# Kernel tuning notes

Measured on AMD Instinct MI355X. Metric: run time of the kernel, lower is better.

## Reference

```python
import jax, jax.numpy as jnp
import numpy as np

D_MODEL = 768; HEADS = 8; LAYERS = 2

def pos_encoding(n, d):
    pos = np.arange(n, dtype=np.float32)[:, None]
    div = np.exp(np.arange(0, d, 2, dtype=np.float32) * -(np.log(10000.0) / d))
    pe = np.zeros((n, d), np.float32)
    pe[:, 0::2] = np.sin(pos * div)
    pe[:, 1::2] = np.cos(pos * div)
    return jnp.asarray(pe)

def layer_norm(x, g, b):
    m = x.mean(-1, keepdims=True)
    v = ((x - m) ** 2).mean(-1, keepdims=True)
    return (x - m) / jnp.sqrt(v + 1e-6) * g + b

def mha(k_in, v_in, q_in, mask, Wq, bq, Wk, bk, Wv, bv, Wout, bout):
    # BertSum MultiHeadedAttention(key, value, query, mask); mask True = blocked
    B, Lq, d = q_in.shape
    dk = d // HEADS
    def proj(x, W, b):
        y = x @ W + b
        return y.reshape(B, x.shape[1], HEADS, dk).transpose(0, 2, 1, 3)
    q = proj(q_in, Wq, bq)
    k = proj(k_in, Wk, bk)
    v = proj(v_in, Wv, bv)
    scores = jnp.einsum('bhqd,bhkd->bhqk', q, k) / jnp.sqrt(jnp.float32(dk))
    scores = jnp.where(mask[:, None, :, :], jnp.float32(-1e18), scores)
    attn = jax.nn.softmax(scores, axis=-1)
    out = jnp.einsum('bhqk,bhkd->bhqd', attn, v).transpose(0, 2, 1, 3).reshape(B, Lq, d)
    return out @ Wout + bout

def ffn(x, W1, b1, W2, b2, g, b):
    # PositionwiseFeedForward: x + w2(gelu(w1(LN(x))))
    return x + jax.nn.gelu(layer_norm(x, g, b) @ W1 + b1) @ W2 + b2

def setup_inputs():
    key = jax.random.key(0)
    ks = jax.random.split(key, 20)
    B, N_TOP, N_OUT, D, DFF, DH = 8, 512, 64, D_MODEL, 3072, 512
    s = 0.02
    return {
        'top_vecs': jax.random.normal(ks[0], (B, N_TOP, D), jnp.float32),
        'inputs': jax.random.normal(ks[1], (B, N_OUT, D), jnp.float32),
        'mask': jnp.ones((B, N_TOP), bool),
        'label_mask': jnp.ones((B, N_OUT), bool),
        'Wq': jax.random.normal(ks[2], (LAYERS, D, D)) * s,
        'bq': jnp.zeros((LAYERS, D)),
        'Wk': jax.random.normal(ks[3], (LAYERS, D, D)) * s,
        'bk': jnp.zeros((LAYERS, D)),
        'Wv': jax.random.normal(ks[4], (LAYERS, D, D)) * s,
        'bv': jnp.zeros((LAYERS, D)),
        'Wout': jax.random.normal(ks[5], (LAYERS, D, D)) * s,
        'bout': jnp.zeros((LAYERS, D)),
        'W1': jax.random.normal(ks[6], (LAYERS, D, DFF)) * s,
        'b1': jnp.zeros((LAYERS, DFF)),
        'W2': jax.random.normal(ks[7], (LAYERS, DFF, D)) * s,
        'b2': jnp.zeros((LAYERS, D)),
        'ln_g': jnp.ones((LAYERS, D)),
        'ln_b': jnp.zeros((LAYERS, D)),
        'Wo': jax.random.normal(ks[8], (D, DH)) * s,
        'bo': jnp.zeros((DH,)),
        'Wi': jax.random.normal(ks[9], (D, DH)) * s,
        'bi': jnp.zeros((DH,)),
        'v_w': jax.random.normal(ks[10], (DH,)) * s,
        'v_b': jnp.zeros(()),
    }

def reference(top_vecs, inputs, mask, label_mask, Wq, bq, Wk, bk, Wv, bv, Wout, bout,
              W1, b1, W2, b2, ln_g, ln_b, Wo, bo, Wi, bi, v_w, v_b):
    B, n_out, d = inputs.shape
    pe = pos_encoding(n_out, d)
    seq_mask = jnp.triu(jnp.ones((n_out, n_out), bool), 1)  # future positions blocked
    self_mask = (~label_mask)[:, None, :] | seq_mask[None]  # (B, n_out, n_out)
    ctx_mask = jnp.broadcast_to((~mask)[:, None, :], (B, n_out, mask.shape[1]))
    x = inputs + pe[None]
    for i in range(LAYERS):
        ctx = mha(x, x, x, self_mask, Wq[i], bq[i], Wk[i], bk[i], Wv[i], bv[i], Wout[i], bout[i])
        dec = mha(top_vecs, top_vecs, ctx, ctx_mask, Wq[i], bq[i], Wk[i], bk[i], Wv[i], bv[i], Wout[i], bout[i])
        x = ffn(dec, W1[i], b1[i], W2[i], b2[i], ln_g[i], ln_b[i])
    # additive-attention scoring head: (B, n_out, n_top, d_hidden) broadcast intermediate
    h = jax.nn.leaky_relu((x @ Wo + bo)[:, :, None, :] + (top_vecs @ Wi + bi)[:, None, :, :])
    scores = jnp.einsum('bonh,h->bon', h, v_w) + v_b
    return jax.nn.softmax(scores, axis=-1)
```

## Files before the change

kernel.cpp:

```cpp
#include <hip/hip_runtime.h>
#include <math.h>

#define D_MODEL 768
#define HEADS   8
#define DK      96
#define NB      8
#define N_TOP   512
#define N_OUT   64
#define DFF     3072
#define DH      512

typedef short  short8  __attribute__((ext_vector_type(8)));
typedef float  floatx4 __attribute__((ext_vector_type(4)));

__device__ __forceinline__ unsigned short f2bf(float f) {
    unsigned int u = __float_as_uint(f);
    u += 0x7fffu + ((u >> 16) & 1u);
    return (unsigned short)(u >> 16);
}
__device__ __forceinline__ float bf2f(unsigned short h) {
    return __uint_as_float(((unsigned int)h) << 16);
}

__device__ __forceinline__ float gelu_f(float x) {
    const float c = 0.7978845608028654f;
    return 0.5f * x * (1.0f + tanhf(c * (x + 0.044715f * x * x * x)));
}

__device__ __forceinline__ void gl16(const short* g, short* l) {
    __builtin_amdgcn_global_load_lds(
        (const __attribute__((address_space(1))) void*)g,
        (__attribute__((address_space(3))) void*)l, 16, 0, 0);
}

__device__ __forceinline__ float block_reduce_sum(float v, float* red) {
    int tid = threadIdx.x;
    red[tid] = v;
    __syncthreads();
    for (int s = blockDim.x >> 1; s > 0; s >>= 1) {
        if (tid < s) red[tid] += red[tid + s];
        __syncthreads();
    }
    float r = red[0];
    __syncthreads();
    return r;
}
__device__ __forceinline__ float block_reduce_max(float v, float* red) {
    int tid = threadIdx.x;
    red[tid] = v;
    __syncthreads();
    for (int s = blockDim.x >> 1; s > 0; s >>= 1) {
        if (tid < s) red[tid] = fmaxf(red[tid], red[tid + s]);
        __syncthreads();
    }
    float r = red[0];
    __syncthreads();
    return r;
}

struct TPack {
    const float* src[14];
    short*       dst[14];
    int K[14], N[14];
    int tstart[15];
};

__global__ __launch_bounds__(256) void multi_transpose_kernel(TPack pk) {
    __shared__ float t[32][33];
    int tile = blockIdx.x;
    int i = 0;
    while (i < 13 && tile >= pk.tstart[i + 1]) ++i;
    int lt = tile - pk.tstart[i];
    int K = pk.K[i], N = pk.N[i];
    int ntx = N >> 5;
    int bx = lt % ntx, by = lt / ntx;
    const float* in = pk.src[i];
    short* out = pk.dst[i];
    int tx = threadIdx.x & 31, ty = threadIdx.x >> 5;
#pragma unroll
    for (int r = 0; r < 4; ++r)
        t[ty + r * 8][tx] = in[(size_t)(by * 32 + ty + r * 8) * N + bx * 32 + tx];
    __syncthreads();
#pragma unroll
    for (int r = 0; r < 4; ++r)
        out[(size_t)(bx * 32 + ty + r * 8) * K + by * 32 + tx] =
            (short)f2bf(t[tx][ty + r * 8]);
}

__global__ void convert_bf16_kernel(const float* __restrict__ in, short* __restrict__ out, int n4) {
    int i = blockIdx.x * blockDim.x + threadIdx.x;
    if (i >= n4) return;
    float4 v = ((const float4*)in)[i];
    out[i * 4 + 0] = (short)f2bf(v.x);
    out[i * 4 + 1] = (short)f2bf(v.y);
    out[i * 4 + 2] = (short)f2bf(v.z);
    out[i * 4 + 3] = (short)f2bf(v.w);
}

__global__ void add_pe_kernel(const float* __restrict__ in, short* __restrict__ xb, int total) {
    int idx = blockIdx.x * blockDim.x + threadIdx.x;
    if (idx >= total) return;
    int c   = idx % D_MODEL;
    int pos = (idx / D_MODEL) % N_OUT;
    int j   = c >> 1;
    float ang = (float)pos * expf((float)(2 * j) * (-logf(10000.0f) / (float)D_MODEL));
    float pe  = (c & 1) ? cosf(ang) : sinf(ang);
    xb[idx] = (short)f2bf(in[idx] + pe);
}

struct GDesc {
    const short* A;
    const short* Bt;
    int K;
    int nbx;
    short*       dst[3];
    const float* bias[3];
    int cum[4];
    int vtlog[3];
    int nseg;
};
struct GPack {
    GDesc d[3];
    int start1, start2;
};

__global__ __launch_bounds__(256) void gemm128g_kernel(GPack gp) {
    __shared__ __align__(16) short As[3 * 128 * 32];
    __shared__ __align__(16) short Bs[3 * 128 * 32];

    const int nwg = gridDim.x, orig = blockIdx.x;
    const int q8 = nwg >> 3, r8 = nwg & 7, xcd = orig & 7, loc = orig >> 3;
    const int blk = (xcd < r8 ? xcd * (q8 + 1) : r8 * (q8 + 1) + (xcd - r8) * q8) + loc;

    const int di = (blk >= gp.start1 ? 1 : 0) + (blk >= gp.start2 ? 1 : 0);
    const GDesc& D = gp.d[di];
    const int l = blk - (di == 0 ? 0 : (di == 1 ? gp.start1 : gp.start2));
    const int bm = (l / D.nbx) * 128, bn = (l % D.nbx) * 128;
    const int K = D.K;
    const int nst = K >> 5;

    const int tid  = threadIdx.x;
    const int wave = tid >> 6, lane = tid & 63;
    const int wr = wave >> 1, wc = wave & 1;
    const int lc = lane & 15;
    const int lq = lane >> 4;
    const int lr4 = lq * 4;
    const int ko  = (lq ^ ((lc >> 1) & 3)) * 8;

    const int srow = wave * 32 + (lane >> 2);
    const int scol = ((lane & 3) ^ ((lane >> 3) & 3)) * 8;
    const int sbase = wave * 1024;

    floatx4 acc[4][4];
#pragma unroll
    for (int i = 0; i < 4; ++i)
#pragma unroll
        for (int j = 0; j < 4; ++j) acc[i][j] = (floatx4)0.0f;

    const short* Ab = D.A  + (size_t)(bm + srow) * K + scol;
    const short* Bb = D.Bt + (size_t)(bn + srow) * K + scol;
    const size_t hq = (size_t)16 * K;

#define STG128(t, buf) do {                                   \
        const short* _a = Ab + (size_t)(t) * 32;              \
        const short* _b = Bb + (size_t)(t) * 32;              \
        short* _la = As + (buf) * 4096 + sbase;               \
        short* _lb = Bs + (buf) * 4096 + sbase;               \
        gl16(_a,      _la);                                   \
        gl16(_a + hq, _la + 512);                             \
        gl16(_b,      _lb);                                   \
        gl16(_b + hq, _lb + 512);                             \
    } while (0)

    STG128(0, 0);
    if (nst > 1) {
        STG128(1, 1);
        asm volatile("s_waitcnt vmcnt(4)" ::: "memory");
    } else {
        asm volatile("s_waitcnt vmcnt(0)" ::: "memory");
    }
    __builtin_amdgcn_s_barrier();

    int cur = 0;
    for (int t = 0; t < nst; ++t) {
        int pre = cur + 2; if (pre >= 3) pre -= 3;
        const bool more = (t + 2) < nst;
        if (more) STG128(t + 2, pre);
        const short* Ar = As + cur * 4096;
        const short* Br = Bs + cur * 4096;
        short8 a[4], b[4];
#pragma unroll
        for (int f = 0; f < 4; ++f) {
            a[f] = *(const short8*)&Ar[(wr * 64 + f * 16 + lc) * 32 + ko];
            b[f] = *(const short8*)&Br[(wc * 64 + f * 16 + lc) * 32 + ko];
        }
#pragma unroll
        for (int fr = 0; fr < 4; ++fr)
#pragma unroll
            for (int fc = 0; fc < 4; ++fc)
                acc[fr][fc] = __builtin_amdgcn_mfma_f32_16x16x32_bf16(
                    a[fr], b[fc], acc[fr][fc], 0, 0, 0);
        if (more) asm volatile("s_waitcnt vmcnt(4)" ::: "memory");
        else      asm volatile("s_waitcnt vmcnt(0)" ::: "memory");
        __builtin_amdgcn_s_barrier();
        if (++cur == 3) cur = 0;
    }
#undef STG128

#pragma unroll
    for (int fc = 0; fc < 4; ++fc) {
        int col = bn + wc * 64 + fc * 16 + lc;
        int s = 0;
        while (s + 1 < D.nseg && col >= D.cum[s + 1]) ++s;
        int cl   = col - D.cum[s];
        int segw = D.cum[s + 1] - D.cum[s];
        const float* bp = D.bias[s];
        short* dst = D.dst[s];
        int vtl = D.vtlog[s];
        float bi = bp ? bp[cl] : 0.0f;
#pragma unroll
        for (int fr = 0; fr < 4; ++fr)
#pragma unroll
            for (int r = 0; r < 4; ++r) {
                int row = bm + wr * 64 + fr * 16 + lr4 + r;
                float x = acc[fr][fc][r] + bi;
                if (vtl) {
                    int seq = 1 << vtl;
                    dst[((size_t)(row >> vtl) * segw + cl) * seq + (row & (seq - 1))] =
                        (short)f2bf(x);
                } else {
                    dst[(size_t)row * segw + cl] = (short)f2bf(x);
                }
            }
    }
}

__global__ __launch_bounds__(256) void gemm_bf16_kernel(
    const short* __restrict__ A, const short* __restrict__ Bt,
    const float* __restrict__ bias0, const float* __restrict__ bias1,
    const float* __restrict__ bias2, const float* __restrict__ residual,
    float* __restrict__ Cf, short* __restrict__ Cb0, short* __restrict__ Cb1,
    short* __restrict__ Cb2,
    int M, int N, int K, int act, int segw, int vt_seg, int vt_log) {
    __shared__ __align__(16) short As[3 * 2 * 64 * 32];
    __shared__ __align__(16) short Bs[3 * 2 * 64 * 32];

    const int gx = gridDim.x, gy = gridDim.y;
    const int nwg = gx * gy;
    const int orig = blockIdx.y * gx + blockIdx.x;
    const int q8 = nwg >> 3, r8 = nwg & 7, xcd = orig & 7, loc = orig >> 3;
    const int wg = (xcd < r8 ? xcd * (q8 + 1) : r8 * (q8 + 1) + (xcd - r8) * q8) + loc;
    const int bm = (wg % gy) * 64, bn = (wg / gy) * 64;

    const int tid  = threadIdx.x;
    const int wave = tid >> 6, lane = tid & 63;
    const int wr = wave >> 1, wc = wave & 1;
    const int lc = lane & 15;
    const int lr4 = (lane >> 4) * 4;
    const int ko  = ((lane >> 4) ^ ((lc >> 1) & 3)) * 8;

    const int srow = wave * 16 + (lane >> 2);
    const int scol = ((lane & 3) ^ ((lane >> 3) & 3)) * 8;
    const int sbase = wave * 512;

    const int nst = K >> 6;

    floatx4 acc[2][2];
#pragma unroll
    for (int i = 0; i < 2; ++i)
#pragma unroll
        for (int j = 0; j < 2; ++j) acc[i][j] = (floatx4)0.0f;

    const short* Ab = A  + (size_t)(bm + srow) * K + scol;
    const short* Bb = Bt + (size_t)(bn + srow) * K + scol;

#define STG64(t, buf) do {                                    \
        const short* _a = Ab + (size_t)(t) * 64;              \
        const short* _b = Bb + (size_t)(t) * 64;              \
        short* _la = As + (buf) * 4096 + sbase;               \
        short* _lb = Bs + (buf) * 4096 + sbase;               \
        gl16(_a,      _la);                                   \
        gl16(_a + 32, _la + 2048);                            \
        gl16(_b,      _lb);                                   \
        gl16(_b + 32, _lb + 2048);                            \
    } while (0)

    STG64(0, 0);
    if (nst > 1) {
        STG64(1, 1);
        asm volatile("s_waitcnt vmcnt(4)" ::: "memory");
    } else {
        asm volatile("s_waitcnt vmcnt(0)" ::: "memory");
    }
    __builtin_amdgcn_s_barrier();

    int cur = 0;
    for (int t = 0; t < nst; ++t) {
        int pre = cur + 2; if (pre >= 3) pre -= 3;
        const bool more = (t + 2) < nst;
        if (more) STG64(t + 2, pre);
#pragma unroll
        for (int sub = 0; sub < 2; ++sub) {
            const short* Ar = As + cur * 4096 + sub * 2048;
            const short* Br = Bs + cur * 4096 + sub * 2048;
            short8 a0 = *(const short8*)&Ar[(wr * 32 + lc) * 32 + ko];
            short8 a1 = *(const short8*)&Ar[(wr * 32 + 16 + lc) * 32 + ko];
            short8 b0 = *(const short8*)&Br[(wc * 32 + lc) * 32 + ko];
            short8 b1 = *(const short8*)&Br[(wc * 32 + 16 + lc) * 32 + ko];
            acc[0][0] = __builtin_amdgcn_mfma_f32_16x16x32_bf16(a0, b0, acc[0][0], 0, 0, 0);
            acc[0][1] = __builtin_amdgcn_mfma_f32_16x16x32_bf16(a0, b1, acc[0][1], 0, 0, 0);
            acc[1][0] = __builtin_amdgcn_mfma_f32_16x16x32_bf16(a1, b0, acc[1][0], 0, 0, 0);
            acc[1][1] = __builtin_amdgcn_mfma_f32_16x16x32_bf16(a1, b1, acc[1][1], 0, 0, 0);
        }
        if (more) asm volatile("s_waitcnt vmcnt(4)" ::: "memory");
        else      asm volatile("s_waitcnt vmcnt(0)" ::: "memory");
        __builtin_amdgcn_s_barrier();
        if (++cur == 3) cur = 0;
    }
#undef STG64

#pragma unroll
    for (int fr = 0; fr < 2; ++fr) {
#pragma unroll
        for (int fc = 0; fc < 2; ++fc) {
            int col = bn + wc * 32 + fc * 16 + lc;
            int seg = (col >= segw) + (col >= 2 * segw);
            int cl  = col - seg * segw;
            const float* bp = (seg == 0) ? bias0 : ((seg == 1) ? bias1 : bias2);
            short* dst      = (seg == 0) ? Cb0   : ((seg == 1) ? Cb1   : Cb2);
            float bi = bp ? bp[cl] : 0.0f;
#pragma unroll
            for (int r = 0; r < 4; ++r) {
                int row = bm + wr * 32 + fr * 16 + lr4 + r;
                float x = acc[fr][fc][r] + bi;
                if (residual) x += residual[(size_t)row * N + col];
                if (act == 1) x = gelu_f(x);
                if (Cf) Cf[(size_t)row * N + col] = x;
                if (dst) {
                    if (seg == vt_seg) {
                        int sq = 1 << vt_log;
                        dst[((size_t)(row >> vt_log) * segw + cl) * sq + (row & (sq - 1))] =
                            (short)f2bf(x);
                    } else {
                        dst[(size_t)row * segw + cl] = (short)f2bf(x);
                    }
                }
            }
        }
    }
}

template<int LK, bool CAUSAL>
__global__ __launch_bounds__(64) void attn_mfma_kernel(
    const short* __restrict__ Q, const short* __restrict__ K,
    const short* __restrict__ VT, short* __restrict__ out) {
    constexpr int NF = LK / 16;
    constexpr int KS = LK / 32;
    __shared__ __align__(16) short P[16][LK + 8];

    int idx = blockIdx.x;
    const int w = idx & 3;  idx >>= 2;
    const int h = idx & 7;  idx >>= 3;
    const int b = idx;
    const int lane = threadIdx.x;
    const int lc = lane & 15;
    const int lq = lane >> 4;
    const int ko = lq * 8;

    short8 qf[3];
    const short* qbase = Q + ((size_t)(b * N_OUT + w * 16 + lc)) * D_MODEL + h * DK;
#pragma unroll
    for (int s = 0; s < 3; ++s) qf[s] = *(const short8*)(qbase + s * 32 + ko);

    floatx4 acc[NF];
#pragma unroll
    for (int f = 0; f < NF; ++f) acc[f] = (floatx4)0.0f;
    const short* kbase = K + ((size_t)(b * LK)) * D_MODEL + h * DK;
#pragma unroll
    for (int f = 0; f < NF; ++f) {
        const short* kr = kbase + (size_t)(f * 16 + lc) * D_MODEL;
#pragma unroll
        for (int s = 0; s < 3; ++s) {
            short8 kf = *(const short8*)(kr + s * 32 + ko);
            acc[f] = __builtin_amdgcn_mfma_f32_16x16x32_bf16(qf[s], kf, acc[f], 0, 0, 0);
        }
    }

    const float scale = 0.10206207261596575f;
    float inv[4];
#pragma unroll
    for (int r = 0; r < 4; ++r) {
        int row = w * 16 + lq * 4 + r;
        float m = -INFINITY;
#pragma unroll
        for (int f = 0; f < NF; ++f) {
            float s = acc[f][r] * scale;
            if (CAUSAL && (f * 16 + lc) > row) s = -INFINITY;
            acc[f][r] = s;
            m = fmaxf(m, s);
        }
#pragma unroll
        for (int d = 1; d < 16; d <<= 1) m = fmaxf(m, __shfl_xor(m, d));
        float sum = 0.0f;
#pragma unroll
        for (int f = 0; f < NF; ++f) {
            float e = expf(acc[f][r] - m);
            acc[f][r] = e;
            sum += e;
        }
#pragma unroll
        for (int d = 1; d < 16; d <<= 1) sum += __shfl_xor(sum, d);
        inv[r] = 1.0f / sum;
    }

#pragma unroll
    for (int f = 0; f < NF; ++f)
#pragma unroll
        for (int r = 0; r < 4; ++r)
            P[lq * 4 + r][f * 16 + lc] = (short)f2bf(acc[f][r] * inv[r]);
    __syncthreads();

    floatx4 oacc[6];
#pragma unroll
    for (int n = 0; n < 6; ++n) oacc[n] = (floatx4)0.0f;
    const short* vbase = VT + ((size_t)b * D_MODEL + h * DK) * LK;
#pragma unroll
    for (int s = 0; s < KS; ++s) {
        short8 pf = *(const short8*)&P[lc][s * 32 + ko];
#pragma unroll
        for (int n = 0; n < 6; ++n) {
            short8 vf = *(const short8*)(vbase + (size_t)(n * 16 + lc) * LK + s * 32 + ko);
            oacc[n] = __builtin_amdgcn_mfma_f32_16x16x32_bf16(pf, vf, oacc[n], 0, 0, 0);
        }
    }

#pragma unroll
    for (int n = 0; n < 6; ++n)
#pragma unroll
        for (int r = 0; r < 4; ++r) {
            int row = b * N_OUT + w * 16 + lq * 4 + r;
            int col = h * DK + n * 16 + lc;
            out[(size_t)row * D_MODEL + col] = (short)f2bf(oacc[n][r]);
        }
}

__global__ __launch_bounds__(256) void layernorm_kernel(
    const float* __restrict__ in, const float* __restrict__ g, const float* __restrict__ b,
    short* __restrict__ out) {
    __shared__ float red[256];
    int row = blockIdx.x, tid = threadIdx.x;
    const float* r = in + (size_t)row * D_MODEL;

    float s = 0.0f;
    for (int c = tid; c < D_MODEL; c += 256) s += r[c];
    float mean = block_reduce_sum(s, red) / (float)D_MODEL;

    float vs = 0.0f;
    for (int c = tid; c < D_MODEL; c += 256) {
        float d = r[c] - mean;
        vs += d * d;
    }
    float var = block_reduce_sum(vs, red) / (float)D_MODEL;
    float inv = 1.0f / sqrtf(var + 1e-6f);

    for (int c = tid; c < D_MODEL; c += 256)
        out[(size_t)row * D_MODEL + c] = (short)f2bf((r[c] - mean) * inv * g[c] + b[c]);
}

__global__ __launch_bounds__(512) void head_kernel(
    const float* __restrict__ a, const short* __restrict__ cb,
    const float* __restrict__ v_w, const float* __restrict__ v_b,
    float* __restrict__ out) {
    __shared__ float as[DH];
    __shared__ float vs[DH];
    __shared__ float red[512];

    int b = blockIdx.x >> 6;
    int o = blockIdx.x & 63;
    int tid = threadIdx.x;

    as[tid] = a[((size_t)b * N_OUT + o) * DH + tid];
    vs[tid] = v_w[tid];
    __syncthreads();

    const short* crow = cb + ((size_t)b * N_TOP + tid) * DH;
    float s0 = 0.0f, s1 = 0.0f, s2 = 0.0f, s3 = 0.0f;
#pragma unroll 2
    for (int hh = 0; hh < DH; hh += 32) {
        short8 c0 = *(const short8*)(crow + hh);
        short8 c1 = *(const short8*)(crow + hh + 8);
        short8 c2 = *(const short8*)(crow + hh + 16);
        short8 c3 = *(const short8*)(crow + hh + 24);
#pragma unroll
        for (int u = 0; u < 8; ++u) {
            float x0 = as[hh + u]      + bf2f((unsigned short)c0[u]);
            float x1 = as[hh + 8 + u]  + bf2f((unsigned short)c1[u]);
            float x2 = as[hh + 16 + u] + bf2f((unsigned short)c2[u]);
            float x3 = as[hh + 24 + u] + bf2f((unsigned short)c3[u]);
            x0 = fmaxf(x0, 0.0f) + 0.01f * fminf(x0, 0.0f);
            x1 = fmaxf(x1, 0.0f) + 0.01f * fminf(x1, 0.0f);
            x2 = fmaxf(x2, 0.0f) + 0.01f * fminf(x2, 0.0f);
            x3 = fmaxf(x3, 0.0f) + 0.01f * fminf(x3, 0.0f);
            s0 = fmaf(vs[hh + u], x0, s0);
            s1 = fmaf(vs[hh + 8 + u], x1, s1);
            s2 = fmaf(vs[hh + 16 + u], x2, s2);
            s3 = fmaf(vs[hh + 24 + u], x3, s3);
        }
    }
    float s = (s0 + s1) + (s2 + s3) + v_b[0];

    float m = block_reduce_max(s, red);
    float e = expf(s - m);
    float sum = block_reduce_sum(e, red);
    out[((size_t)b * N_OUT + o) * N_TOP + tid] = e / sum;
}

extern "C" void kernel_launch(void* const* d_in, const int* in_sizes, int n_in,
                              void* d_out, int out_size, void* d_ws, size_t ws_size,
                              hipStream_t stream) {
    const float* top  = (const float*)d_in[0];
    const float* inp  = (const float*)d_in[1];
    const float* Wq   = (const float*)d_in[4];
    const float* bq   = (const float*)d_in[5];
    const float* Wk   = (const float*)d_in[6];
    const float* bk   = (const float*)d_in[7];
    const float* Wv   = (const float*)d_in[8];
    const float* bv   = (const float*)d_in[9];
    const float* Wout = (const float*)d_in[10];
    const float* bout = (const float*)d_in[11];
    const float* W1   = (const float*)d_in[12];
    const float* b1   = (const float*)d_in[13];
    const float* W2   = (const float*)d_in[14];
    const float* b2   = (const float*)d_in[15];
    const float* ln_g = (const float*)d_in[16];
    const float* ln_b = (const float*)d_in[17];
    const float* Wo   = (const float*)d_in[18];
    const float* bo   = (const float*)d_in[19];
    const float* Wi   = (const float*)d_in[20];
    const float* bi   = (const float*)d_in[21];
    const float* v_w  = (const float*)d_in[22];
    const float* v_b  = (const float*)d_in[23];

    char* p = (char*)d_ws;
    auto alloc = [&](size_t bytes) -> void* {
        void* r = (void*)p;
        p += (bytes + 255) & ~(size_t)255;
        return r;
    };

    const size_t WSQ = 768 * 768;
    short *WT_q[2], *WT_k[2], *WT_v[2], *WT_o[2], *WT_1[2], *WT_2[2];
    for (int L = 0; L < 2; ++L) {
        WT_q[L] = (short*)alloc(WSQ * 2);
        WT_k[L] = (short*)alloc(WSQ * 2);
        WT_v[L] = (short*)alloc(WSQ * 2);
        WT_o[L] = (short*)alloc(WSQ * 2);
        WT_1[L] = (short*)alloc((size_t)768 * DFF * 2);
        WT_2[L] = (short*)alloc((size_t)768 * DFF * 2);
    }
    short* WT_oh = (short*)alloc((size_t)768 * DH * 2);
    short* WT_ih = (short*)alloc((size_t)768 * DH * 2);

    const int NX  = NB * N_OUT * D_MODEL;
    const int NKV = NB * N_TOP * D_MODEL;

    short* top_bf = (short*)alloc((size_t)NKV * 2);
    short* X_bf   = (short*)alloc((size_t)NX * 2);
    short* Q_bf   = (short*)alloc((size_t)NX * 2);
    short* K_bf   = (short*)alloc((size_t)NKV * 2);
    short* VT     = (short*)alloc((size_t)NKV * 2);
    short* AO_bf  = (short*)alloc((size_t)NX * 2);
    short* CTX_bf = (short*)alloc((size_t)NX * 2);
    float* DEC    = (float*)alloc((size_t)NX * 4);
    short* LNO_bf = (short*)alloc((size_t)NX * 2);
    short* MID_bf = (short*)alloc((size_t)NB * N_OUT * DFF * 2);
    float* a_h    = (float*)alloc((size_t)NB * N_OUT * DH * 4);
    short* c_hb   = (short*)alloc((size_t)NB * N_TOP * DH * 2);

    TPack pk;
    {
        int i = 0, t = 0;
        auto put = [&](const float* s, short* d, int K, int N) {
            pk.src[i] = s; pk.dst[i] = d; pk.K[i] = K; pk.N[i] = N;
            pk.tstart[i] = t; t += (K / 32) * (N / 32); ++i;
        };
        for (int L = 0; L < 2; ++L) {
            put(Wq + (size_t)L * WSQ, WT_q[L], 768, 768);
            put(Wk + (size_t)L * WSQ, WT_k[L], 768, 768);
            put(Wv + (size_t)L * WSQ, WT_v[L], 768, 768);
            put(Wout + (size_t)L * WSQ, WT_o[L], 768, 768);
            put(W1 + (size_t)L * 768 * DFF, WT_1[L], 768, DFF);
            put(W2 + (size_t)L * DFF * 768, WT_2[L], DFF, 768);
        }
        put(Wo, WT_oh, 768, DH);
        put(Wi, WT_ih, 768, DH);
        pk.tstart[14] = t;
        hipLaunchKernelGGL(multi_transpose_kernel, dim3(t), dim3(256), 0, stream, pk);
    }

    hipLaunchKernelGGL(convert_bf16_kernel, dim3(NKV / 4 / 256), dim3(256), 0, stream,
                       top, top_bf, NKV / 4);
    hipLaunchKernelGGL(add_pe_kernel, dim3((NX + 255) / 256), dim3(256), 0, stream,
                       inp, X_bf, NX);

    const int MQ = NB * N_OUT;
    const int MT = NB * N_TOP;

    auto G = [&](const short* A, const short* Bt,
                 const float* b0, const float* b1p, const float* b2p,
                 const float* res, float* Cf, short* C0, short* C1, short* C2,
                 int M, int N, int K, int act, int segw, int vt_seg, int vt_log) {
        hipLaunchKernelGGL(gemm_bf16_kernel, dim3(N / 64, M / 64), dim3(256), 0, stream,
                           A, Bt, b0, b1p, b2p, res, Cf, C0, C1, C2,
                           M, N, K, act, segw, vt_seg, vt_log);
    };

    for (int L = 0; L < 2; ++L) {
        const float* _bq = bq + (size_t)L * D_MODEL;
        const float* _bk = bk + (size_t)L * D_MODEL;
        const float* _bv = bv + (size_t)L * D_MODEL;
        const float* _bo = bout + (size_t)L * D_MODEL;
        const float* _b1 = b1 + (size_t)L * DFF;
        const float* _b2 = b2 + (size_t)L * D_MODEL;
        const float* _g  = ln_g + (size_t)L * D_MODEL;
        const float* _b  = ln_b + (size_t)L * D_MODEL;

        {
            GPack gp{};
            gp.d[0].A = top_bf; gp.d[0].Bt = WT_k[L]; gp.d[0].K = D_MODEL;
            gp.d[0].nbx = 1536 / 128;
            gp.d[0].dst[0] = K_bf; gp.d[0].bias[0] = _bk; gp.d[0].vtlog[0] = 0;
            gp.d[0].dst[1] = VT;   gp.d[0].bias[1] = _bv; gp.d[0].vtlog[1] = 9;
            gp.d[0].cum[0] = 0; gp.d[0].cum[1] = 768; gp.d[0].cum[2] = 1536;
            gp.d[0].nseg = 2;
            int nb0 = (MT / 128) * gp.d[0].nbx;
            gp.d[1].A = X_bf; gp.d[1].Bt = WT_q[L]; gp.d[1].K = D_MODEL;
            gp.d[1].nbx = 2304 / 128;
            gp.d[1].dst[0] = Q_bf;   gp.d[1].bias[0] = _bq; gp.d[1].vtlog[0] = 0;
            gp.d[1].dst[1] = LNO_bf; gp.d[1].bias[1] = _bk; gp.d[1].vtlog[1] = 0;
            gp.d[1].dst[2] = MID_bf; gp.d[1].bias[2] = _bv; gp.d[1].vtlog[2] = 6;
            gp.d[1].cum[0] = 0; gp.d[1].cum[1] = 768; gp.d[1].cum[2] = 1536;
            gp.d[1].cum[3] = 2304; gp.d[1].nseg = 3;
            int nb1 = (MQ / 128) * gp.d[1].nbx;
            gp.start1 = nb0;
            int total = nb0 + nb1;
            if (L == 0) {
                gp.d[2].A = top_bf; gp.d[2].Bt = WT_ih; gp.d[2].K = D_MODEL;
                gp.d[2].nbx = DH / 128;
                gp.d[2].dst[0] = c_hb; gp.d[2].bias[0] = bi; gp.d[2].vtlog[0] = 0;
                gp.d[2].cum[0] = 0; gp.d[2].cum[1] = DH; gp.d[2].nseg = 1;
                gp.start2 = total;
                total += (MT / 128) * gp.d[2].nbx;
            } else {
                gp.start2 = 1 << 30;
            }
            hipLaunchKernelGGL(gemm128g_kernel, dim3(total), dim3(256), 0, stream, gp);
        }

        hipLaunchKernelGGL((attn_mfma_kernel<64, true>), dim3(NB * HEADS * 4), dim3(64),
                           0, stream, Q_bf, LNO_bf, MID_bf, AO_bf);
        G(AO_bf, WT_o[L], _bo, nullptr, nullptr, nullptr, nullptr, CTX_bf, nullptr, nullptr,
          MQ, D_MODEL, D_MODEL, 0, D_MODEL, -1, 0);

        G(CTX_bf, WT_q[L], _bq, nullptr, nullptr, nullptr, nullptr, Q_bf, nullptr, nullptr,
          MQ, D_MODEL, D_MODEL, 0, D_MODEL, -1, 0);
        hipLaunchKernelGGL((attn_mfma_kernel<512, false>), dim3(NB * HEADS * 4), dim3(64),
                           0, stream, Q_bf, K_bf, VT, AO_bf);
        G(AO_bf, WT_o[L], _bo, nullptr, nullptr, nullptr, DEC, nullptr, nullptr, nullptr,
          MQ, D_MODEL, D_MODEL, 0, D_MODEL, -1, 0);

        hipLaunchKernelGGL(layernorm_kernel, dim3(MQ), dim3(256), 0, stream,
                           DEC, _g, _b, LNO_bf);
        G(LNO_bf, WT_1[L], _b1, nullptr, nullptr, nullptr, nullptr, MID_bf, nullptr, nullptr,
          MQ, DFF, D_MODEL, 1, DFF, -1, 0);
        G(MID_bf, WT_2[L], _b2, nullptr, nullptr, DEC, nullptr, X_bf, nullptr, nullptr,
          MQ, D_MODEL, DFF, 0, D_MODEL, -1, 0);
    }

    G(X_bf, WT_oh, bo, nullptr, nullptr, nullptr, a_h, nullptr, nullptr, nullptr,
      MQ, DH, D_MODEL, 0, DH, -1, 0);
    hipLaunchKernelGGL(head_kernel, dim3(NB * N_OUT), dim3(512), 0, stream,
                       a_h, c_hb, v_w, v_b, (float*)d_out);
}
```

Baseline: 530.7 us.

## Add split-K to small GEMMs and switch to double-buffered LDS pipeline

Adds split-K (grid z) to the small-M GEMMs (out-projections, Q projection, FFN down projection, head projection). Each split writes fp32 partials, and a new combine kernel adds bias and residual and writes fp32 or bf16. This gives more workgroups to fill the GPU on GEMMs with few output tiles. Separately, both GEMM kernels drop from a triple-buffered LDS pipeline with explicit vmcnt waits to double buffering with __syncthreads, which cuts LDS use but may expose more load latency. The change also adds an extra launch and partial-buffer traffic per split GEMM.

```diff
diff --git a/kernel.cpp b/kernel.cpp
--- a/kernel.cpp
+++ b/kernel.cpp
@@ -11,6 +11,7 @@
 #define DH      512
 
 typedef short  short8  __attribute__((ext_vector_type(8)));
+typedef short  short4v __attribute__((ext_vector_type(4)));
 typedef float  floatx4 __attribute__((ext_vector_type(4)));
 
 __device__ __forceinline__ unsigned short f2bf(float f) {
@@ -125,8 +126,8 @@
 };
 
 __global__ __launch_bounds__(256) void gemm128g_kernel(GPack gp) {
-    __shared__ __align__(16) short As[3 * 128 * 32];
-    __shared__ __align__(16) short Bs[3 * 128 * 32];
+    __shared__ __align__(16) short As[2 * 128 * 32];
+    __shared__ __align__(16) short Bs[2 * 128 * 32];
 
     const int nwg = gridDim.x, orig = blockIdx.x;
     const int q8 = nwg >> 3, r8 = nwg & 7, xcd = orig & 7, loc = orig >> 3;
@@ -173,19 +174,11 @@
     } while (0)
 
     STG128(0, 0);
-    if (nst > 1) {
-        STG128(1, 1);
-        asm volatile("s_waitcnt vmcnt(4)" ::: "memory");
-    } else {
-        asm volatile("s_waitcnt vmcnt(0)" ::: "memory");
-    }
-    __builtin_amdgcn_s_barrier();
+    __syncthreads();
 
     int cur = 0;
     for (int t = 0; t < nst; ++t) {
-        int pre = cur + 2; if (pre >= 3) pre -= 3;
-        const bool more = (t + 2) < nst;
-        if (more) STG128(t + 2, pre);
+        if (t + 1 < nst) STG128(t + 1, cur ^ 1);
         const short* Ar = As + cur * 4096;
         const short* Br = Bs + cur * 4096;
         short8 a[4], b[4];
@@ -200,10 +193,8 @@
             for (int fc = 0; fc < 4; ++fc)
                 acc[fr][fc] = __builtin_amdgcn_mfma_f32_16x16x32_bf16(
                     a[fr], b[fc], acc[fr][fc], 0, 0, 0);
-        if (more) asm volatile("s_waitcnt vmcnt(4)" ::: "memory");
-        else      asm volatile("s_waitcnt vmcnt(0)" ::: "memory");
-        __builtin_amdgcn_s_barrier();
-        if (++cur == 3) cur = 0;
+        __syncthreads();
+        cur ^= 1;
     }
 #undef STG128
 
@@ -240,10 +231,10 @@
     const float* __restrict__ bias0, const float* __restrict__ bias1,
     const float* __restrict__ bias2, const float* __restrict__ residual,
     float* __restrict__ Cf, short* __restrict__ Cb0, short* __restrict__ Cb1,
-    short* __restrict__ Cb2,
+    short* __restrict__ Cb2, float* __restrict__ part,
     int M, int N, int K, int act, int segw, int vt_seg, int vt_log) {
-    __shared__ __align__(16) short As[3 * 2 * 64 * 32];
-    __shared__ __align__(16) short Bs[3 * 2 * 64 * 32];
+    __shared__ __align__(16) short As[2 * 2 * 64 * 32];
+    __shared__ __align__(16) short Bs[2 * 2 * 64 * 32];
 
     const int gx = gridDim.x, gy = gridDim.y;
     const int nwg = gx * gy;
@@ -252,6 +243,9 @@
     const int wg = (xcd < r8 ? xcd * (q8 + 1) : r8 * (q8 + 1) + (xcd - r8) * q8) + loc;
     const int bm = (wg % gy) * 64, bn = (wg / gy) * 64;
 
+    const int nz = gridDim.z, kz = blockIdx.z;
+    const int kchunk = K / nz;
+
     const int tid  = threadIdx.x;
     const int wave = tid >> 6, lane = tid & 63;
     const int wr = wave >> 1, wc = wave & 1;
@@ -263,7 +257,7 @@
     const int scol = ((lane & 3) ^ ((lane >> 3) & 3)) * 8;
     const int sbase = wave * 512;
 
-    const int nst = K >> 6;
+    const int nst = kchunk >> 6;
 
     floatx4 acc[2][2];
 #pragma unroll
@@ -271,8 +265,8 @@
 #pragma unroll
         for (int j = 0; j < 2; ++j) acc[i][j] = (floatx4)0.0f;
 
-    const short* Ab = A  + (size_t)(bm + srow) * K + scol;
-    const short* Bb = Bt + (size_t)(bn + srow) * K + scol;
+    const short* Ab = A  + (size_t)(bm + srow) * K + kz * kchunk + scol;
+    const short* Bb = Bt + (size_t)(bn + srow) * K + kz * kchunk + scol;
 
 #define STG64(t, buf) do {                                    \
         const short* _a = Ab + (size_t)(t) * 64;              \
@@ -286,19 +280,11 @@
     } while (0)
 
     STG64(0, 0);
-    if (nst > 1) {
-        STG64(1, 1);
-        asm volatile("s_waitcnt vmcnt(4)" ::: "memory");
-    } else {
-        asm volatile("s_waitcnt vmcnt(0)" ::: "memory");
-    }
-    __builtin_amdgcn_s_barrier();
+    __syncthreads();
 
     int cur = 0;
     for (int t = 0; t < nst; ++t) {
-        int pre = cur + 2; if (pre >= 3) pre -= 3;
-        const bool more = (t + 2) < nst;
-        if (more) STG64(t + 2, pre);
+        if (t + 1 < nst) STG64(t + 1, cur ^ 1);
 #pragma unroll
         for (int sub = 0; sub < 2; ++sub) {
             const short* Ar = As + cur * 4096 + sub * 2048;
@@ -312,12 +298,26 @@
             acc[1][0] = __builtin_amdgcn_mfma_f32_16x16x32_bf16(a1, b0, acc[1][0], 0, 0, 0);
             acc[1][1] = __builtin_amdgcn_mfma_f32_16x16x32_bf16(a1, b1, acc[1][1], 0, 0, 0);
         }
-        if (more) asm volatile("s_waitcnt vmcnt(4)" ::: "memory");
-        else      asm volatile("s_waitcnt vmcnt(0)" ::: "memory");
-        __builtin_amdgcn_s_barrier();
-        if (++cur == 3) cur = 0;
+        __syncthreads();
+        cur ^= 1;
     }
 #undef STG64
+
+    if (nz > 1) {
+        float* pt = part + (size_t)kz * M * N;
+#pragma unroll
+        for (int fr = 0; fr < 2; ++fr)
+#pragma unroll
+            for (int fc = 0; fc < 2; ++fc) {
+                int col = bn + wc * 32 + fc * 16 + lc;
+#pragma unroll
+                for (int r = 0; r < 4; ++r) {
+                    int row = bm + wr * 32 + fr * 16 + lr4 + r;
+                    pt[(size_t)row * N + col] = acc[fr][fc][r];
+                }
+            }
+        return;
+    }
 
 #pragma unroll
     for (int fr = 0; fr < 2; ++fr) {
@@ -347,6 +347,32 @@
                 }
             }
         }
+    }
+}
+
+__global__ __launch_bounds__(256) void combine_kernel(
+    const float* __restrict__ part, int nz, int N, int MN,
+    const float* __restrict__ bias, const float* __restrict__ residual,
+    float* __restrict__ Cf, short* __restrict__ Cb) {
+    int e = (blockIdx.x * 256 + threadIdx.x) * 4;
+    float4 s = *(const float4*)(part + e);
+    for (int z = 1; z < nz; ++z) {
+        float4 p = *(const float4*)(part + (size_t)z * MN + e);
+        s.x += p.x; s.y += p.y; s.z += p.z; s.w += p.w;
+    }
+    int col = e % N;
+    float4 b4 = *(const float4*)(bias + col);
+    s.x += b4.x; s.y += b4.y; s.z += b4.z; s.w += b4.w;
+    if (residual) {
+        float4 r4 = *(const float4*)(residual + e);
+        s.x += r4.x; s.y += r4.y; s.z += r4.z; s.w += r4.w;
+    }
+    if (Cf) *(float4*)(Cf + e) = s;
+    if (Cb) {
+        short4v o;
+        o[0] = (short)f2bf(s.x); o[1] = (short)f2bf(s.y);
+        o[2] = (short)f2bf(s.z); o[3] = (short)f2bf(s.w);
+        *(short4v*)(Cb + e) = o;
     }
 }
 
@@ -576,6 +602,7 @@
     short* MID_bf = (short*)alloc((size_t)NB * N_OUT * DFF * 2);
     float* a_h    = (float*)alloc((size_t)NB * N_OUT * DH * 4);
     short* c_hb   = (short*)alloc((size_t)NB * N_TOP * DH * 2);
+    float* PART   = (float*)alloc((size_t)4 * NX * 4);
 
     TPack pk;
     {
@@ -607,12 +634,21 @@
     const int MT = NB * N_TOP;
 
     auto G = [&](const short* A, const short* Bt,
-                 const float* b0, const float* b1p, const float* b2p,
-                 const float* res, float* Cf, short* C0, short* C1, short* C2,
-                 int M, int N, int K, int act, int segw, int vt_seg, int vt_log) {
-        hipLaunchKernelGGL(gemm_bf16_kernel, dim3(N / 64, M / 64), dim3(256), 0, stream,
-                           A, Bt, b0, b1p, b2p, res, Cf, C0, C1, C2,
-                           M, N, K, act, segw, vt_seg, vt_log);
+                 const float* b0, const float* res, float* Cf, short* C0,
+                 int M, int N, int K, int act) {
+        hipLaunchKernelGGL(gemm_bf16_kernel, dim3(N / 64, M / 64, 1), dim3(256), 0, stream,
+                           A, Bt, b0, nullptr, nullptr, res, Cf, C0, nullptr, nullptr,
+                           nullptr, M, N, K, act, N, -1, 0);
+    };
+    auto GS = [&](const short* A, const short* Bt, const float* b0,
+                  const float* res, float* Cf, short* C0,
+                  int M, int N, int K, int nz) {
+        hipLaunchKernelGGL(gemm_bf16_kernel, dim3(N / 64, M / 64, nz), dim3(256), 0, stream,
+                           A, Bt, nullptr, nullptr, nullptr, nullptr,
+                           nullptr, nullptr, nullptr, nullptr, PART,
+                           M, N, K, 0, N, -1, 0);
+        hipLaunchKernelGGL(combine_kernel, dim3(M * N / 1024), dim3(256), 0, stream,
+                           PART, nz, N, M * N, b0, res, Cf, C0);
     };
 
     for (int L = 0; L < 2; ++L) {
@@ -659,26 +695,20 @@
 
         hipLaunchKernelGGL((attn_mfma_kernel<64, true>), dim3(NB * HEADS * 4), dim3(64),
                            0, stream, Q_bf, LNO_bf, MID_bf, AO_bf);
-        G(AO_bf, WT_o[L], _bo, nullptr, nullptr, nullptr, nullptr, CTX_bf, nullptr, nullptr,
-          MQ, D_MODEL, D_MODEL, 0, D_MODEL, -1, 0);
-
-        G(CTX_bf, WT_q[L], _bq, nullptr, nullptr, nullptr, nullptr, Q_bf, nullptr, nullptr,
-          MQ, D_MODEL, D_MODEL, 0, D_MODEL, -1, 0);
+        GS(AO_bf, WT_o[L], _bo, nullptr, nullptr, CTX_bf, MQ, D_MODEL, D_MODEL, 3);
+
+        GS(CTX_bf, WT_q[L], _bq, nullptr, nullptr, Q_bf, MQ, D_MODEL, D_MODEL, 3);
         hipLaunchKernelGGL((attn_mfma_kernel<512, false>), dim3(NB * HEADS * 4), dim3(64),
                            0, stream, Q_bf, K_bf, VT, AO_bf);
-        G(AO_bf, WT_o[L], _bo, nullptr, nullptr, nullptr, DEC, nullptr, nullptr, nullptr,
-          MQ, D_MODEL, D_MODEL, 0, D_MODEL, -1, 0);
+        GS(AO_bf, WT_o[L], _bo, nullptr, DEC, nullptr, MQ, D_MODEL, D_MODEL, 3);
 
         hipLaunchKernelGGL(layernorm_kernel, dim3(MQ), dim3(256), 0, stream,
                            DEC, _g, _b, LNO_bf);
-        G(LNO_bf, WT_1[L], _b1, nullptr, nullptr, nullptr, nullptr, MID_bf, nullptr, nullptr,
-          MQ, DFF, D_MODEL, 1, DFF, -1, 0);
-        G(MID_bf, WT_2[L], _b2, nullptr, nullptr, DEC, nullptr, X_bf, nullptr, nullptr,
-          MQ, D_MODEL, DFF, 0, D_MODEL, -1, 0);
-    }
-
-    G(X_bf, WT_oh, bo, nullptr, nullptr, nullptr, a_h, nullptr, nullptr, nullptr,
-      MQ, DH, D_MODEL, 0, DH, -1, 0);
+        G(LNO_bf, WT_1[L], _b1, nullptr, nullptr, MID_bf, MQ, DFF, D_MODEL, 1);
+        GS(MID_bf, WT_2[L], _b2, DEC, nullptr, X_bf, MQ, D_MODEL, DFF, 4);
+    }
+
+    GS(X_bf, WT_oh, bo, nullptr, a_h, nullptr, MQ, DH, D_MODEL, 3);
     hipLaunchKernelGGL(head_kernel, dim3(NB * N_OUT), dim3(512), 0, stream,
                        a_h, c_hb, v_w, v_b, (float*)d_out);
 }
```

Result: faster. 481.0 us (-9.4%).
